# Optimization experiments

Measured on AMD Instinct MI355X. Metric: run time of the kernel, lower is better.

Reference implementation:

```python
import jax, jax.numpy as jnp
import numpy as np

N_LAYERS = 3
N_NODES = 512
D_IN = 4  # dimensions + 1
BATCH = 131072


def _glorot(key, shape):
    fan_in, fan_out = shape[-2], shape[-1]
    lim = np.sqrt(6.0 / (fan_in + fan_out))
    return jax.random.uniform(key, shape, jnp.float32, -lim, lim)


def setup_inputs() -> dict:
    key = jax.random.key(0)
    ks = jax.random.split(key, 12)
    L, n, d = N_LAYERS, N_NODES, D_IN
    return {
        "X": jax.random.normal(ks[0], (BATCH, d), jnp.float32),
        "W_in": _glorot(ks[1], (d, n)),
        "b_in": jnp.zeros((1, n), jnp.float32),
        "Wf": _glorot(ks[2], (L, d, n)),
        "Uf": _glorot(ks[3], (L, n, n)),
        "bf": jnp.zeros((L, 1, n), jnp.float32),
        "Wu": _glorot(ks[4], (L, d, n)),
        "Uu": _glorot(ks[5], (L, n, n)),
        "bu": jnp.zeros((L, 1, n), jnp.float32),
        "Wo1": _glorot(ks[6], (L, d, n)),
        "Uo1": _glorot(ks[7], (L, n, n)),
        "bo1": jnp.zeros((L, 1, n), jnp.float32),
        "Wo2": _glorot(ks[8], (L, n, n)),
        "bo2": jnp.zeros((L, 1, n), jnp.float32),
        "W_out": _glorot(ks[9], (n, 1)),
        "b_out": jnp.zeros((1, 1), jnp.float32),
    }


def reference(X, W_in, b_in, Wf, Uf, bf, Wu, Uu, bu, Wo1, Uo1, bo1, Wo2, bo2, W_out, b_out):
    # initial dense layer with swish activation
    H = jax.nn.silu(X @ W_in + b_in)  # [B, n_nodes]
    for i in range(N_LAYERS):
        F = jax.nn.sigmoid(X @ Wf[i] + H @ Uf[i] + bf[i])
        U = jax.nn.sigmoid(X @ Wu[i] + H @ Uu[i] + bu[i])
        O1 = jnp.tanh(X @ Wo1[i] + H @ Uo1[i] + bo1[i])
        O2 = jax.nn.silu((U * O1) @ Wo2[i] + bo2[i])
        H = F * H + O2
    return jax.nn.silu(H @ W_out + b_out)  # [B, 1]
```

## Files before the change

### kernel.cpp

```cpp
#include <hip/hip_runtime.h>
#include <cstdint>
#include <cstddef>

#define NLAYERS 3
#define NN      512
#define DIN     4
#define MTILE   64
#define KAUG    544
#define LDA     552
#define WELEMS  (NN * KAUG)
#define LDS_BYTES (2 * MTILE * LDA * 2)
#define NTHREADS 1024

typedef __attribute__((ext_vector_type(8))) short short8;
typedef __attribute__((ext_vector_type(4))) float f32x4;

__device__ __forceinline__ short f2bf(float f) {
    union { float f; uint32_t u; } v; v.f = f;
    uint32_t r = v.u + 0x7fffu + ((v.u >> 16) & 1u);
    return (short)(r >> 16);
}
__device__ __forceinline__ uint32_t f2bf_pk(float lo, float hi) {
    uint32_t r;
    asm("v_cvt_pk_bf16_f32 %0, %1, %2" : "=v"(r) : "v"(lo), "v"(hi));
    return r;
}
__device__ __forceinline__ float bf2f(short s) {
    union { uint32_t u; float f; } v; v.u = ((uint32_t)(uint16_t)s) << 16;
    return v.f;
}
__device__ __forceinline__ float sig_(float x)  { return 1.0f / (1.0f + __expf(-x)); }
__device__ __forceinline__ float tanh_(float x) { return 1.0f - 2.0f / (1.0f + __expf(2.0f * x)); }
__device__ __forceinline__ float silu_(float x) { return x / (1.0f + __expf(-x)); }

__device__ __forceinline__ void sig2_(float a, float b, float& sa, float& sb) {
    float da = 1.0f + __expf(-a);
    float db = 1.0f + __expf(-b);
    float inv = 1.0f / (da * db);
    sa = db * inv;
    sb = da * inv;
}
__device__ __forceinline__ void tanh2_(float a, float b, float& ta, float& tb) {
    float da = 1.0f + __expf(2.0f * a);
    float db = 1.0f + __expf(2.0f * b);
    float inv = 1.0f / (da * db);
    ta = 1.0f - 2.0f * (db * inv);
    tb = 1.0f - 2.0f * (da * inv);
}
__device__ __forceinline__ void silu2_(float a, float b, float& sa, float& sb) {
    float da = 1.0f + __expf(-a);
    float db = 1.0f + __expf(-b);
    float inv = 1.0f / (da * db);
    sa = a * (db * inv);
    sb = b * (da * inv);
}

#define MFMA_BF16 __builtin_amdgcn_mfma_f32_16x16x32_bf16

__global__ void prep_kernel(const float* __restrict__ Wf,  const float* __restrict__ Uf,  const float* __restrict__ bf,
                            const float* __restrict__ Wu,  const float* __restrict__ Uu,  const float* __restrict__ bu,
                            const float* __restrict__ Wo1, const float* __restrict__ Uo1, const float* __restrict__ bo1,
                            const float* __restrict__ Wo2, const float* __restrict__ bo2,
                            short* __restrict__ ws) {
    int idx = blockIdx.x * 256 + threadIdx.x;
    int m   = idx / WELEMS;
    if (m >= 12) return;
    int rem = idx - m * WELEMS;
    int n   = rem / KAUG;
    int kk  = rem - n * KAUG;
    int layer = m >> 2, t = m & 3;
    const float* U; const float* W; const float* b;
    switch (t) {
        case 0:  U = Uf;  W = Wf;      b = bf;  break;
        case 1:  U = Uu;  W = Wu;      b = bu;  break;
        case 2:  U = Uo1; W = Wo1;     b = bo1; break;
        default: U = Wo2; W = nullptr; b = bo2; break;
    }
    float val = 0.0f;
    if (kk < NN)             val = U[layer * NN * NN + kk * NN + n];
    else if (kk < NN + DIN)  val = W ? W[layer * DIN * NN + (kk - NN) * NN + n] : 0.0f;
    else if (kk == NN + DIN) val = b[layer * NN + n];
    ws[idx] = f2bf(val);
}

__device__ __forceinline__ void mm1(const short* __restrict__ Asrc, const short* __restrict__ Bt,
                                    int n0, int l16, int quad, f32x4 (&acc)[4][2]) {
#pragma unroll
    for (int mt = 0; mt < 4; ++mt)
#pragma unroll
        for (int nt = 0; nt < 2; ++nt) acc[mt][nt] = f32x4{0.f, 0.f, 0.f, 0.f};
    const short* aP = Asrc + l16 * LDA + quad * 8;
    const short* bP = Bt + (size_t)(n0 + l16) * KAUG + quad * 8;

    short8 a0[4], a1[4];
    short8 b0[2], b1[2];

#pragma unroll
    for (int mt = 0; mt < 4; ++mt) a0[mt] = *(const short8*)(aP + mt * 16 * LDA);
#pragma unroll
    for (int nt = 0; nt < 2; ++nt) {
        b0[nt] = *(const short8*)(bP + nt * 16 * KAUG);
        b1[nt] = *(const short8*)(bP + nt * 16 * KAUG + 32);
    }

#pragma unroll 1
    for (int i = 0; i < 7; ++i) {
#pragma unroll
        for (int mt = 0; mt < 4; ++mt) a1[mt] = *(const short8*)(aP + mt * 16 * LDA + 32);
#pragma unroll
        for (int mt = 0; mt < 4; ++mt) {
            acc[mt][0] = MFMA_BF16(a0[mt], b0[0], acc[mt][0], 0, 0, 0);
            acc[mt][1] = MFMA_BF16(a0[mt], b0[1], acc[mt][1], 0, 0, 0);
        }
#pragma unroll
        for (int nt = 0; nt < 2; ++nt) b0[nt] = *(const short8*)(bP + nt * 16 * KAUG + 64);
#pragma unroll
        for (int mt = 0; mt < 4; ++mt) a0[mt] = *(const short8*)(aP + mt * 16 * LDA + 64);
#pragma unroll
        for (int mt = 0; mt < 4; ++mt) {
            acc[mt][0] = MFMA_BF16(a1[mt], b1[0], acc[mt][0], 0, 0, 0);
            acc[mt][1] = MFMA_BF16(a1[mt], b1[1], acc[mt][1], 0, 0, 0);
        }
#pragma unroll
        for (int nt = 0; nt < 2; ++nt) b1[nt] = *(const short8*)(bP + nt * 16 * KAUG + 96);
        aP += 64; bP += 64;
    }
#pragma unroll
    for (int mt = 0; mt < 4; ++mt) a1[mt] = *(const short8*)(aP + mt * 16 * LDA + 32);
#pragma unroll
    for (int mt = 0; mt < 4; ++mt) {
        acc[mt][0] = MFMA_BF16(a0[mt], b0[0], acc[mt][0], 0, 0, 0);
        acc[mt][1] = MFMA_BF16(a0[mt], b0[1], acc[mt][1], 0, 0, 0);
    }
#pragma unroll
    for (int nt = 0; nt < 2; ++nt) b0[nt] = *(const short8*)(bP + nt * 16 * KAUG + 64);
#pragma unroll
    for (int mt = 0; mt < 4; ++mt) a0[mt] = *(const short8*)(aP + mt * 16 * LDA + 64);
#pragma unroll
    for (int mt = 0; mt < 4; ++mt) {
        acc[mt][0] = MFMA_BF16(a1[mt], b1[0], acc[mt][0], 0, 0, 0);
        acc[mt][1] = MFMA_BF16(a1[mt], b1[1], acc[mt][1], 0, 0, 0);
    }
#pragma unroll
    for (int mt = 0; mt < 4; ++mt) {
        acc[mt][0] = MFMA_BF16(a0[mt], b0[0], acc[mt][0], 0, 0, 0);
        acc[mt][1] = MFMA_BF16(a0[mt], b0[1], acc[mt][1], 0, 0, 0);
    }
}

__global__ void __launch_bounds__(NTHREADS, 4)
dgm_kernel(const float* __restrict__ X, const float* __restrict__ W_in, const float* __restrict__ b_in,
           const float* __restrict__ W_out, const float* __restrict__ b_out,
           const short* __restrict__ wmats, float* __restrict__ out) {
    extern __shared__ short lds[];
    short* Hb = lds;
    short* Tb = lds + MTILE * LDA;

    const int tid  = threadIdx.x;
    const int lane = tid & 63;
    const int wv   = tid >> 6;
    const int l16  = lane & 15;
    const int quad = lane >> 4;
    const int n0   = wv * 32;
    const int rbase = blockIdx.x * MTILE;

    {
        const int cfix = tid & (NN - 1);
        const int rstart = tid >> 9;
        const float w0 = W_in[0 * NN + cfix];
        const float w1 = W_in[1 * NN + cfix];
        const float w2 = W_in[2 * NN + cfix];
        const float w3 = W_in[3 * NN + cfix];
        const float bc = b_in[cfix];
#pragma unroll 4
        for (int j = 0; j < (MTILE * NN) / NTHREADS; ++j) {
            int r = rstart + j * (NTHREADS / NN);
            const float4 x = *(const float4*)(X + (size_t)(rbase + r) * DIN);
            float v = bc + x.x * w0 + x.y * w1 + x.z * w2 + x.w * w3;
            Hb[r * LDA + cfix] = f2bf(silu_(v));
        }
    }
    if (tid < MTILE) {
        int r = tid;
        const float* xr = X + (size_t)(rbase + r) * DIN;
#pragma unroll
        for (int k = 0; k < DIN; ++k) {
            Hb[r * LDA + NN + k] = f2bf(xr[k]);
            Tb[r * LDA + NN + k] = 0;
        }
        Hb[r * LDA + NN + DIN] = f2bf(1.0f);
        Tb[r * LDA + NN + DIN] = f2bf(1.0f);
        for (int k = NN + DIN + 1; k < KAUG; ++k) {
            Hb[r * LDA + k] = 0;
            Tb[r * LDA + k] = 0;
        }
    }
    __syncthreads();

    uint32_t Fpack[16];

    for (int layer = 0; layer < NLAYERS; ++layer) {
        const short* wF  = wmats + (size_t)(layer * 4 + 0) * WELEMS;
        const short* wU  = wmats + (size_t)(layer * 4 + 1) * WELEMS;
        const short* wO1 = wmats + (size_t)(layer * 4 + 2) * WELEMS;
        const short* wO2 = wmats + (size_t)(layer * 4 + 3) * WELEMS;

        uint32_t Tpack[16];
        {
            f32x4 aO[4][2];
            mm1(Hb, wO1, n0, l16, quad, aO);
#pragma unroll
            for (int mt = 0; mt < 4; ++mt)
#pragma unroll
                for (int nt = 0; nt < 2; ++nt)
#pragma unroll
                    for (int rp = 0; rp < 2; ++rp) {
                        float t0, t1;
                        tanh2_(aO[mt][nt][2 * rp + 0], aO[mt][nt][2 * rp + 1], t0, t1);
                        Tpack[mt * 4 + nt * 2 + rp] = f2bf_pk(t0, t1);
                    }
        }
        {
            f32x4 aU[4][2];
            mm1(Hb, wU, n0, l16, quad, aU);
#pragma unroll
            for (int mt = 0; mt < 4; ++mt)
#pragma unroll
                for (int nt = 0; nt < 2; ++nt)
#pragma unroll
                    for (int rp = 0; rp < 2; ++rp) {
                        uint32_t tp = Tpack[mt * 4 + nt * 2 + rp];
                        float to0 = bf2f((short)(uint16_t)(tp & 0xffffu));
                        float to1 = bf2f((short)(uint16_t)(tp >> 16));
                        float s0, s1;
                        sig2_(aU[mt][nt][2 * rp + 0], aU[mt][nt][2 * rp + 1], s0, s1);
                        uint32_t pk = f2bf_pk(s0 * to0, s1 * to1);
                        int row = mt * 16 + quad * 4 + 2 * rp;
                        int col = n0 + nt * 16 + l16;
                        Tb[row * LDA + col]       = (short)(uint16_t)(pk & 0xffffu);
                        Tb[(row + 1) * LDA + col] = (short)(uint16_t)(pk >> 16);
                    }
        }
        {
            f32x4 aF[4][2];
            mm1(Hb, wF, n0, l16, quad, aF);
#pragma unroll
            for (int mt = 0; mt < 4; ++mt)
#pragma unroll
                for (int nt = 0; nt < 2; ++nt)
#pragma unroll
                    for (int rp = 0; rp < 2; ++rp) {
                        float s0, s1;
                        sig2_(aF[mt][nt][2 * rp + 0], aF[mt][nt][2 * rp + 1], s0, s1);
                        Fpack[mt * 4 + nt * 2 + rp] = f2bf_pk(s0, s1);
                    }
        }
        __syncthreads();

        {
            f32x4 aO2[4][2];
            mm1(Tb, wO2, n0, l16, quad, aO2);
#pragma unroll
            for (int mt = 0; mt < 4; ++mt)
#pragma unroll
                for (int nt = 0; nt < 2; ++nt)
#pragma unroll
                    for (int rp = 0; rp < 2; ++rp) {
                        uint32_t fp = Fpack[mt * 4 + nt * 2 + rp];
                        float f0 = bf2f((short)(uint16_t)(fp & 0xffffu));
                        float f1 = bf2f((short)(uint16_t)(fp >> 16));
                        int row = mt * 16 + quad * 4 + 2 * rp;
                        int col = n0 + nt * 16 + l16;
                        float h0 = bf2f(Hb[row * LDA + col]);
                        float h1 = bf2f(Hb[(row + 1) * LDA + col]);
                        float sl0, sl1;
                        silu2_(aO2[mt][nt][2 * rp + 0], aO2[mt][nt][2 * rp + 1], sl0, sl1);
                        uint32_t pk = f2bf_pk(f0 * h0 + sl0, f1 * h1 + sl1);
                        Hb[row * LDA + col]       = (short)(uint16_t)(pk & 0xffffu);
                        Hb[(row + 1) * LDA + col] = (short)(uint16_t)(pk >> 16);
                    }
        }
        __syncthreads();
    }

    {
        const int r = tid >> 4, q = tid & 15;
        const int c0 = q * (NN / 16);
        const short8* hp = (const short8*)(Hb + r * LDA + c0);
        float p = 0.0f;
#pragma unroll
        for (int v = 0; v < (NN / 16) / 8; ++v) {
            short8 h = hp[v];
#pragma unroll
            for (int e = 0; e < 8; ++e)
                p += bf2f(h[e]) * W_out[c0 + v * 8 + e];
        }
        float* red = (float*)Tb;
        red[tid] = p;
        __syncthreads();
        if (q == 0) {
            float s = b_out[0];
#pragma unroll
            for (int i = 0; i < 16; ++i) s += red[r * 16 + i];
            out[rbase + r] = silu_(s);
        }
    }
}

extern "C" void kernel_launch(void* const* d_in, const int* in_sizes, int n_in,
                              void* d_out, int out_size, void* d_ws, size_t ws_size,
                              hipStream_t stream) {
    const float* X     = (const float*)d_in[0];
    const float* W_in  = (const float*)d_in[1];
    const float* b_in  = (const float*)d_in[2];
    const float* Wf    = (const float*)d_in[3];
    const float* Uf    = (const float*)d_in[4];
    const float* bf    = (const float*)d_in[5];
    const float* Wu    = (const float*)d_in[6];
    const float* Uu    = (const float*)d_in[7];
    const float* bu    = (const float*)d_in[8];
    const float* Wo1   = (const float*)d_in[9];
    const float* Uo1   = (const float*)d_in[10];
    const float* bo1   = (const float*)d_in[11];
    const float* Wo2   = (const float*)d_in[12];
    const float* bo2   = (const float*)d_in[13];
    const float* W_out = (const float*)d_in[14];
    const float* b_out = (const float*)d_in[15];
    float* out = (float*)d_out;
    short* ws  = (short*)d_ws;

    const int B = in_sizes[0] / DIN;

    prep_kernel<<<(12 * WELEMS + 255) / 256, 256, 0, stream>>>(
        Wf, Uf, bf, Wu, Uu, bu, Wo1, Uo1, bo1, Wo2, bo2, ws);

    hipFuncSetAttribute((const void*)dgm_kernel,
                        hipFuncAttributeMaxDynamicSharedMemorySize, LDS_BYTES);
    dgm_kernel<<<B / MTILE, NTHREADS, LDS_BYTES, stream>>>(X, W_in, b_in, W_out, b_out, ws, out);
}
```

Baseline: 1.197 ms.

## Split fused DGM kernel into per-layer global-memory GEMM kernels without LDS

Replaces the single fused kernel, which kept the H and T tiles in LDS, with a sequence of kernels: an H init kernel, three GEMM kernels per layer (U/O1 gate, F gate, O2 plus state update) and an output kernel. Activations now travel through bf16 global buffers in the workspace, and A operands are read straight from global memory. Without LDS, each kernel can have higher occupancy (launch bounds of 4). The cost is heavy extra global traffic for activations, many more kernel launches, and a dependence on the workspace size, with the old fused kernel kept as a fallback.

After: 1.177 ms. Within noise of the previous version (-1.6%).

```diff
diff --git a/kernel.cpp b/kernel.cpp
--- a/kernel.cpp
+++ b/kernel.cpp
@@ -7,6 +7,7 @@
 #define DIN     4
 #define MTILE   64
 #define KAUG    544
+#define KA      560
 #define LDA     552
 #define WELEMS  (NN * KAUG)
 #define LDS_BYTES (2 * MTILE * LDA * 2)
@@ -32,27 +33,23 @@
 __device__ __forceinline__ float sig_(float x)  { return 1.0f / (1.0f + __expf(-x)); }
 __device__ __forceinline__ float tanh_(float x) { return 1.0f - 2.0f / (1.0f + __expf(2.0f * x)); }
 __device__ __forceinline__ float silu_(float x) { return x / (1.0f + __expf(-x)); }
-
 __device__ __forceinline__ void sig2_(float a, float b, float& sa, float& sb) {
     float da = 1.0f + __expf(-a);
     float db = 1.0f + __expf(-b);
     float inv = 1.0f / (da * db);
-    sa = db * inv;
-    sb = da * inv;
+    sa = db * inv; sb = da * inv;
 }
 __device__ __forceinline__ void tanh2_(float a, float b, float& ta, float& tb) {
     float da = 1.0f + __expf(2.0f * a);
     float db = 1.0f + __expf(2.0f * b);
     float inv = 1.0f / (da * db);
-    ta = 1.0f - 2.0f * (db * inv);
-    tb = 1.0f - 2.0f * (da * inv);
+    ta = 1.0f - 2.0f * (db * inv); tb = 1.0f - 2.0f * (da * inv);
 }
 __device__ __forceinline__ void silu2_(float a, float b, float& sa, float& sb) {
     float da = 1.0f + __expf(-a);
     float db = 1.0f + __expf(-b);
     float inv = 1.0f / (da * db);
-    sa = a * (db * inv);
-    sb = b * (da * inv);
+    sa = a * (db * inv); sb = b * (da * inv);
 }
 
 #define MFMA_BF16 __builtin_amdgcn_mfma_f32_16x16x32_bf16
@@ -81,6 +78,290 @@
     else if (kk < NN + DIN)  val = W ? W[layer * DIN * NN + (kk - NN) * NN + n] : 0.0f;
     else if (kk == NN + DIN) val = b[layer * NN + n];
     ws[idx] = f2bf(val);
+}
+
+
+__device__ __forceinline__ void mm1g(const short* __restrict__ Asrc, const short* __restrict__ Bt,
+                                     int n0, int l16, int quad, f32x4 (&acc)[4][2]) {
+#pragma unroll
+    for (int mt = 0; mt < 4; ++mt)
+#pragma unroll
+        for (int nt = 0; nt < 2; ++nt) acc[mt][nt] = f32x4{0.f, 0.f, 0.f, 0.f};
+    const short* aP = Asrc + l16 * KA + quad * 8;
+    const short* bP = Bt + (size_t)(n0 + l16) * KAUG + quad * 8;
+
+    short8 a0[4], a1[4];
+    short8 b0[2], b1[2];
+
+#pragma unroll
+    for (int mt = 0; mt < 4; ++mt) a0[mt] = *(const short8*)(aP + mt * 16 * KA);
+#pragma unroll
+    for (int nt = 0; nt < 2; ++nt) {
+        b0[nt] = *(const short8*)(bP + nt * 16 * KAUG);
+        b1[nt] = *(const short8*)(bP + nt * 16 * KAUG + 32);
+    }
+
+#pragma unroll 1
+    for (int i = 0; i < 7; ++i) {
+#pragma unroll
+        for (int mt = 0; mt < 4; ++mt) a1[mt] = *(const short8*)(aP + mt * 16 * KA + 32);
+#pragma unroll
+        for (int mt = 0; mt < 4; ++mt) {
+            acc[mt][0] = MFMA_BF16(a0[mt], b0[0], acc[mt][0], 0, 0, 0);
+            acc[mt][1] = MFMA_BF16(a0[mt], b0[1], acc[mt][1], 0, 0, 0);
+        }
+#pragma unroll
+        for (int nt = 0; nt < 2; ++nt) b0[nt] = *(const short8*)(bP + nt * 16 * KAUG + 64);
+#pragma unroll
+        for (int mt = 0; mt < 4; ++mt) a0[mt] = *(const short8*)(aP + mt * 16 * KA + 64);
+#pragma unroll
+        for (int mt = 0; mt < 4; ++mt) {
+            acc[mt][0] = MFMA_BF16(a1[mt], b1[0], acc[mt][0], 0, 0, 0);
+            acc[mt][1] = MFMA_BF16(a1[mt], b1[1], acc[mt][1], 0, 0, 0);
+        }
+#pragma unroll
+        for (int nt = 0; nt < 2; ++nt) b1[nt] = *(const short8*)(bP + nt * 16 * KAUG + 96);
+        aP += 64; bP += 64;
+    }
+#pragma unroll
+    for (int mt = 0; mt < 4; ++mt) a1[mt] = *(const short8*)(aP + mt * 16 * KA + 32);
+#pragma unroll
+    for (int mt = 0; mt < 4; ++mt) {
+        acc[mt][0] = MFMA_BF16(a0[mt], b0[0], acc[mt][0], 0, 0, 0);
+        acc[mt][1] = MFMA_BF16(a0[mt], b0[1], acc[mt][1], 0, 0, 0);
+    }
+#pragma unroll
+    for (int nt = 0; nt < 2; ++nt) b0[nt] = *(const short8*)(bP + nt * 16 * KAUG + 64);
+#pragma unroll
+    for (int mt = 0; mt < 4; ++mt) a0[mt] = *(const short8*)(aP + mt * 16 * KA + 64);
+#pragma unroll
+    for (int mt = 0; mt < 4; ++mt) {
+        acc[mt][0] = MFMA_BF16(a1[mt], b1[0], acc[mt][0], 0, 0, 0);
+        acc[mt][1] = MFMA_BF16(a1[mt], b1[1], acc[mt][1], 0, 0, 0);
+    }
+#pragma unroll
+    for (int mt = 0; mt < 4; ++mt) {
+        acc[mt][0] = MFMA_BF16(a0[mt], b0[0], acc[mt][0], 0, 0, 0);
+        acc[mt][1] = MFMA_BF16(a0[mt], b0[1], acc[mt][1], 0, 0, 0);
+    }
+}
+
+__device__ __forceinline__ void mmUO1g(const short* __restrict__ Asrc,
+                                       const short* __restrict__ BtU, const short* __restrict__ BtO,
+                                       int n0, int l16, int quad,
+                                       f32x4 (&accU)[4][2], f32x4 (&accO)[4][2]) {
+#pragma unroll
+    for (int mt = 0; mt < 4; ++mt)
+#pragma unroll
+        for (int nt = 0; nt < 2; ++nt) {
+            accU[mt][nt] = f32x4{0.f, 0.f, 0.f, 0.f};
+            accO[mt][nt] = f32x4{0.f, 0.f, 0.f, 0.f};
+        }
+    const short* aP  = Asrc + l16 * KA + quad * 8;
+    const short* bUP = BtU + (size_t)(n0 + l16) * KAUG + quad * 8;
+    const short* bOP = BtO + (size_t)(n0 + l16) * KAUG + quad * 8;
+
+    short8 a[4];
+    short8 bU0[2], bU1[2], bO0[2], bO1[2];
+
+#pragma unroll
+    for (int mt = 0; mt < 4; ++mt) a[mt] = *(const short8*)(aP + mt * 16 * KA);
+#pragma unroll
+    for (int nt = 0; nt < 2; ++nt) {
+        bU0[nt] = *(const short8*)(bUP + nt * 16 * KAUG);
+        bU1[nt] = *(const short8*)(bUP + nt * 16 * KAUG + 32);
+        bO0[nt] = *(const short8*)(bOP + nt * 16 * KAUG);
+        bO1[nt] = *(const short8*)(bOP + nt * 16 * KAUG + 32);
+    }
+
+#pragma unroll 1
+    for (int i = 0; i < 8; ++i) {
+#pragma unroll
+        for (int mt = 0; mt < 4; ++mt) {
+            accU[mt][0] = MFMA_BF16(a[mt], bU0[0], accU[mt][0], 0, 0, 0);
+            accU[mt][1] = MFMA_BF16(a[mt], bU0[1], accU[mt][1], 0, 0, 0);
+            accO[mt][0] = MFMA_BF16(a[mt], bO0[0], accO[mt][0], 0, 0, 0);
+            accO[mt][1] = MFMA_BF16(a[mt], bO0[1], accO[mt][1], 0, 0, 0);
+            a[mt] = *(const short8*)(aP + mt * 16 * KA + 32);
+        }
+#pragma unroll
+        for (int nt = 0; nt < 2; ++nt) {
+            bU0[nt] = *(const short8*)(bUP + nt * 16 * KAUG + 64);
+            bO0[nt] = *(const short8*)(bOP + nt * 16 * KAUG + 64);
+        }
+#pragma unroll
+        for (int mt = 0; mt < 4; ++mt) {
+            accU[mt][0] = MFMA_BF16(a[mt], bU1[0], accU[mt][0], 0, 0, 0);
+            accU[mt][1] = MFMA_BF16(a[mt], bU1[1], accU[mt][1], 0, 0, 0);
+            accO[mt][0] = MFMA_BF16(a[mt], bO1[0], accO[mt][0], 0, 0, 0);
+            accO[mt][1] = MFMA_BF16(a[mt], bO1[1], accO[mt][1], 0, 0, 0);
+            a[mt] = *(const short8*)(aP + mt * 16 * KA + 64);
+        }
+#pragma unroll
+        for (int nt = 0; nt < 2; ++nt) {
+            bU1[nt] = *(const short8*)(bUP + nt * 16 * KAUG + 96);
+            bO1[nt] = *(const short8*)(bOP + nt * 16 * KAUG + 96);
+        }
+        aP += 64; bUP += 64; bOP += 64;
+    }
+#pragma unroll
+    for (int mt = 0; mt < 4; ++mt) {
+        accU[mt][0] = MFMA_BF16(a[mt], bU0[0], accU[mt][0], 0, 0, 0);
+        accU[mt][1] = MFMA_BF16(a[mt], bU0[1], accU[mt][1], 0, 0, 0);
+        accO[mt][0] = MFMA_BF16(a[mt], bO0[0], accO[mt][0], 0, 0, 0);
+        accO[mt][1] = MFMA_BF16(a[mt], bO0[1], accO[mt][1], 0, 0, 0);
+    }
+}
+
+__global__ void __launch_bounds__(NTHREADS)
+hinit_kernel(const float* __restrict__ X, const float* __restrict__ W_in, const float* __restrict__ b_in,
+             short* __restrict__ Hg, short* __restrict__ Tg) {
+    const int tid = threadIdx.x;
+    const int rbase = blockIdx.x * MTILE;
+    {
+        const int cfix = tid & (NN - 1);
+        const int rstart = tid >> 9;
+        const float w0 = W_in[0 * NN + cfix];
+        const float w1 = W_in[1 * NN + cfix];
+        const float w2 = W_in[2 * NN + cfix];
+        const float w3 = W_in[3 * NN + cfix];
+        const float bc = b_in[cfix];
+#pragma unroll 4
+        for (int j = 0; j < (MTILE * NN) / NTHREADS; ++j) {
+            int r = rstart + j * (NTHREADS / NN);
+            const float4 x = *(const float4*)(X + (size_t)(rbase + r) * DIN);
+            float v = bc + x.x * w0 + x.y * w1 + x.z * w2 + x.w * w3;
+            Hg[(size_t)(rbase + r) * KA + cfix] = f2bf(silu_(v));
+        }
+    }
+    if (tid < MTILE) {
+        int r = rbase + tid;
+        const float* xr = X + (size_t)r * DIN;
+#pragma unroll
+        for (int k = 0; k < DIN; ++k) {
+            Hg[(size_t)r * KA + NN + k] = f2bf(xr[k]);
+            Tg[(size_t)r * KA + NN + k] = 0;
+        }
+        Hg[(size_t)r * KA + NN + DIN] = f2bf(1.0f);
+        Tg[(size_t)r * KA + NN + DIN] = f2bf(1.0f);
+        for (int k = NN + DIN + 1; k < KAUG; ++k) {
+            Hg[(size_t)r * KA + k] = 0;
+            Tg[(size_t)r * KA + k] = 0;
+        }
+    }
+}
+
+__global__ void __launch_bounds__(NTHREADS, 4)
+gemm_t_kernel(const short* __restrict__ Hg, const short* __restrict__ wU, const short* __restrict__ wO1,
+              short* __restrict__ Tg) {
+    const int tid  = threadIdx.x;
+    const int lane = tid & 63;
+    const int wv   = tid >> 6;
+    const int l16  = lane & 15;
+    const int quad = lane >> 4;
+    const int n0   = wv * 32;
+    const int rbase = blockIdx.x * MTILE;
+
+    f32x4 aU[4][2], aO[4][2];
+    mmUO1g(Hg + (size_t)rbase * KA, wU, wO1, n0, l16, quad, aU, aO);
+#pragma unroll
+    for (int mt = 0; mt < 4; ++mt)
+#pragma unroll
+        for (int nt = 0; nt < 2; ++nt)
+#pragma unroll
+            for (int rp = 0; rp < 2; ++rp) {
+                float t0, t1, s0, s1;
+                tanh2_(aO[mt][nt][2 * rp + 0], aO[mt][nt][2 * rp + 1], t0, t1);
+                sig2_(aU[mt][nt][2 * rp + 0], aU[mt][nt][2 * rp + 1], s0, s1);
+                uint32_t pk = f2bf_pk(s0 * t0, s1 * t1);
+                int row = rbase + mt * 16 + quad * 4 + 2 * rp;
+                int col = n0 + nt * 16 + l16;
+                Tg[(size_t)row * KA + col]       = (short)(uint16_t)(pk & 0xffffu);
+                Tg[(size_t)(row + 1) * KA + col] = (short)(uint16_t)(pk >> 16);
+            }
+}
+
+__global__ void __launch_bounds__(NTHREADS, 4)
+gemm_f_kernel(const short* __restrict__ Hg, const short* __restrict__ wF, short* __restrict__ Fg) {
+    const int tid  = threadIdx.x;
+    const int lane = tid & 63;
+    const int wv   = tid >> 6;
+    const int l16  = lane & 15;
+    const int quad = lane >> 4;
+    const int n0   = wv * 32;
+    const int rbase = blockIdx.x * MTILE;
+
+    f32x4 aF[4][2];
+    mm1g(Hg + (size_t)rbase * KA, wF, n0, l16, quad, aF);
+#pragma unroll
+    for (int mt = 0; mt < 4; ++mt)
+#pragma unroll
+        for (int nt = 0; nt < 2; ++nt)
+#pragma unroll
+            for (int rp = 0; rp < 2; ++rp) {
+                float s0, s1;
+                sig2_(aF[mt][nt][2 * rp + 0], aF[mt][nt][2 * rp + 1], s0, s1);
+                uint32_t pk = f2bf_pk(s0, s1);
+                int row = rbase + mt * 16 + quad * 4 + 2 * rp;
+                int col = n0 + nt * 16 + l16;
+                Fg[(size_t)row * NN + col]       = (short)(uint16_t)(pk & 0xffffu);
+                Fg[(size_t)(row + 1) * NN + col] = (short)(uint16_t)(pk >> 16);
+            }
+}
+
+__global__ void __launch_bounds__(NTHREADS, 4)
+gemm_h_kernel(const short* __restrict__ Tg, const short* __restrict__ wO2,
+              const short* __restrict__ Fg, short* __restrict__ Hg) {
+    const int tid  = threadIdx.x;
+    const int lane = tid & 63;
+    const int wv   = tid >> 6;
+    const int l16  = lane & 15;
+    const int quad = lane >> 4;
+    const int n0   = wv * 32;
+    const int rbase = blockIdx.x * MTILE;
+
+    f32x4 aO2[4][2];
+    mm1g(Tg + (size_t)rbase * KA, wO2, n0, l16, quad, aO2);
+#pragma unroll
+    for (int mt = 0; mt < 4; ++mt)
+#pragma unroll
+        for (int nt = 0; nt < 2; ++nt)
+#pragma unroll
+            for (int rp = 0; rp < 2; ++rp) {
+                int row = rbase + mt * 16 + quad * 4 + 2 * rp;
+                int col = n0 + nt * 16 + l16;
+                float f0 = bf2f(Fg[(size_t)row * NN + col]);
+                float f1 = bf2f(Fg[(size_t)(row + 1) * NN + col]);
+                float h0 = bf2f(Hg[(size_t)row * KA + col]);
+                float h1 = bf2f(Hg[(size_t)(row + 1) * KA + col]);
+                float sl0, sl1;
+                silu2_(aO2[mt][nt][2 * rp + 0], aO2[mt][nt][2 * rp + 1], sl0, sl1);
+                uint32_t pk = f2bf_pk(f0 * h0 + sl0, f1 * h1 + sl1);
+                Hg[(size_t)row * KA + col]       = (short)(uint16_t)(pk & 0xffffu);
+                Hg[(size_t)(row + 1) * KA + col] = (short)(uint16_t)(pk >> 16);
+            }
+}
+
+__global__ void __launch_bounds__(NTHREADS)
+out_kernel(const short* __restrict__ Hg, const float* __restrict__ W_out, const float* __restrict__ b_out,
+           float* __restrict__ outp) {
+    const int tid = threadIdx.x;
+    const int q = tid & 15;
+    const int row = blockIdx.x * MTILE + (tid >> 4);
+    const short8* hp = (const short8*)(Hg + (size_t)row * KA + q * 32);
+    float p = 0.0f;
+#pragma unroll
+    for (int v = 0; v < 4; ++v) {
+        short8 h = hp[v];
+#pragma unroll
+        for (int e = 0; e < 8; ++e)
+            p += bf2f(h[e]) * W_out[q * 32 + v * 8 + e];
+    }
+    p += __shfl_xor(p, 8, 16);
+    p += __shfl_xor(p, 4, 16);
+    p += __shfl_xor(p, 2, 16);
+    p += __shfl_xor(p, 1, 16);
+    if (q == 0) outp[row] = silu_(p + b_out[0]);
 }
 
 __device__ __forceinline__ void mm1(const short* __restrict__ Asrc, const short* __restrict__ Bt,
@@ -334,7 +615,28 @@
     prep_kernel<<<(12 * WELEMS + 255) / 256, 256, 0, stream>>>(
         Wf, Uf, bf, Wu, Uu, bu, Wo1, Uo1, bo1, Wo2, bo2, ws);
 
-    hipFuncSetAttribute((const void*)dgm_kernel,
-                        hipFuncAttributeMaxDynamicSharedMemorySize, LDS_BYTES);
-    dgm_kernel<<<B / MTILE, NTHREADS, LDS_BYTES, stream>>>(X, W_in, b_in, W_out, b_out, ws, out);
-}
+    const size_t need = 2ull * (12ull * WELEMS + 2ull * (size_t)B * KA + (size_t)B * NN);
+
+    if (ws_size >= need && (B % MTILE) == 0) {
+        short* Hg = ws + 12ull * WELEMS;
+        short* Tg = Hg + (size_t)B * KA;
+        short* Fg = Tg + (size_t)B * KA;
+        const int G = B / MTILE;
+
+        hinit_kernel<<<G, NTHREADS, 0, stream>>>(X, W_in, b_in, Hg, Tg);
+        for (int layer = 0; layer < NLAYERS; ++layer) {
+            const short* wF  = ws + (size_t)(layer * 4 + 0) * WELEMS;
+            const short* wU  = ws + (size_t)(layer * 4 + 1) * WELEMS;
+            const short* wO1 = ws + (size_t)(layer * 4 + 2) * WELEMS;
+            const short* wO2 = ws + (size_t)(layer * 4 + 3) * WELEMS;
+            gemm_t_kernel<<<G, NTHREADS, 0, stream>>>(Hg, wU, wO1, Tg);
+            gemm_f_kernel<<<G, NTHREADS, 0, stream>>>(Hg, wF, Fg);
+            gemm_h_kernel<<<G, NTHREADS, 0, stream>>>(Tg, wO2, Fg, Hg);
+        }
+        out_kernel<<<G, NTHREADS, 0, stream>>>(Hg, W_out, b_out, out);
+    } else {
+        hipFuncSetAttribute((const void*)dgm_kernel,
+                            hipFuncAttributeMaxDynamicSharedMemorySize, LDS_BYTES);
+        dgm_kernel<<<B / MTILE, NTHREADS, LDS_BYTES, stream>>>(X, W_in, b_in, W_out, b_out, ws, out);
+    }
+}
```

## Halve row tile to 32 with 8 waves each covering 64 output columns

Applied to the files above, without the earlier changes.

Shrinks the per-block row tile from 64 to 32 and the block from 1024 to 512 threads, so each wave now computes 32 rows by 64 columns instead of 64 rows by 32. This halves LDS per block and doubles the grid, which may raise occupancy. Each wave now loads more weight fragments from global/L2 per MFMA (4 B tiles per 2 A tiles). Total weight traffic doubles because twice as many blocks each stream all layer weights.

Result: slower. 1.811 ms (+51.4%).

```diff
diff --git a/kernel.cpp b/kernel.cpp
--- a/kernel.cpp
+++ b/kernel.cpp
@@ -5,12 +5,12 @@
 #define NLAYERS 3
 #define NN      512
 #define DIN     4
-#define MTILE   64
+#define MTILE   32
 #define KAUG    544
 #define LDA     552
 #define WELEMS  (NN * KAUG)
 #define LDS_BYTES (2 * MTILE * LDA * 2)
-#define NTHREADS 1024
+#define NTHREADS 512
 
 typedef __attribute__((ext_vector_type(8))) short short8;
 typedef __attribute__((ext_vector_type(4))) float f32x4;
@@ -32,27 +32,23 @@
 __device__ __forceinline__ float sig_(float x)  { return 1.0f / (1.0f + __expf(-x)); }
 __device__ __forceinline__ float tanh_(float x) { return 1.0f - 2.0f / (1.0f + __expf(2.0f * x)); }
 __device__ __forceinline__ float silu_(float x) { return x / (1.0f + __expf(-x)); }
-
 __device__ __forceinline__ void sig2_(float a, float b, float& sa, float& sb) {
     float da = 1.0f + __expf(-a);
     float db = 1.0f + __expf(-b);
     float inv = 1.0f / (da * db);
-    sa = db * inv;
-    sb = da * inv;
+    sa = db * inv; sb = da * inv;
 }
 __device__ __forceinline__ void tanh2_(float a, float b, float& ta, float& tb) {
     float da = 1.0f + __expf(2.0f * a);
     float db = 1.0f + __expf(2.0f * b);
     float inv = 1.0f / (da * db);
-    ta = 1.0f - 2.0f * (db * inv);
-    tb = 1.0f - 2.0f * (da * inv);
+    ta = 1.0f - 2.0f * (db * inv); tb = 1.0f - 2.0f * (da * inv);
 }
 __device__ __forceinline__ void silu2_(float a, float b, float& sa, float& sb) {
     float da = 1.0f + __expf(-a);
     float db = 1.0f + __expf(-b);
     float inv = 1.0f / (da * db);
-    sa = a * (db * inv);
-    sb = b * (da * inv);
+    sa = a * (db * inv); sb = b * (da * inv);
 }
 
 #define MFMA_BF16 __builtin_amdgcn_mfma_f32_16x16x32_bf16
@@ -84,21 +80,21 @@
 }
 
 __device__ __forceinline__ void mm1(const short* __restrict__ Asrc, const short* __restrict__ Bt,
-                                    int n0, int l16, int quad, f32x4 (&acc)[4][2]) {
-#pragma unroll
-    for (int mt = 0; mt < 4; ++mt)
-#pragma unroll
-        for (int nt = 0; nt < 2; ++nt) acc[mt][nt] = f32x4{0.f, 0.f, 0.f, 0.f};
+                                    int n0, int l16, int quad, f32x4 (&acc)[2][4]) {
+#pragma unroll
+    for (int mt = 0; mt < 2; ++mt)
+#pragma unroll
+        for (int nt = 0; nt < 4; ++nt) acc[mt][nt] = f32x4{0.f, 0.f, 0.f, 0.f};
     const short* aP = Asrc + l16 * LDA + quad * 8;
     const short* bP = Bt + (size_t)(n0 + l16) * KAUG + quad * 8;
 
-    short8 a0[4], a1[4];
-    short8 b0[2], b1[2];
-
-#pragma unroll
-    for (int mt = 0; mt < 4; ++mt) a0[mt] = *(const short8*)(aP + mt * 16 * LDA);
-#pragma unroll
-    for (int nt = 0; nt < 2; ++nt) {
+    short8 a0[2], a1[2];
+    short8 b0[4], b1[4];
+
+#pragma unroll
+    for (int mt = 0; mt < 2; ++mt) a0[mt] = *(const short8*)(aP + mt * 16 * LDA);
+#pragma unroll
+    for (int nt = 0; nt < 4; ++nt) {
         b0[nt] = *(const short8*)(bP + nt * 16 * KAUG);
         b1[nt] = *(const short8*)(bP + nt * 16 * KAUG + 32);
     }
@@ -106,46 +102,46 @@
 #pragma unroll 1
     for (int i = 0; i < 7; ++i) {
 #pragma unroll
-        for (int mt = 0; mt < 4; ++mt) a1[mt] = *(const short8*)(aP + mt * 16 * LDA + 32);
-#pragma unroll
-        for (int mt = 0; mt < 4; ++mt) {
-            acc[mt][0] = MFMA_BF16(a0[mt], b0[0], acc[mt][0], 0, 0, 0);
-            acc[mt][1] = MFMA_BF16(a0[mt], b0[1], acc[mt][1], 0, 0, 0);
-        }
-#pragma unroll
-        for (int nt = 0; nt < 2; ++nt) b0[nt] = *(const short8*)(bP + nt * 16 * KAUG + 64);
-#pragma unroll
-        for (int mt = 0; mt < 4; ++mt) a0[mt] = *(const short8*)(aP + mt * 16 * LDA + 64);
-#pragma unroll
-        for (int mt = 0; mt < 4; ++mt) {
-            acc[mt][0] = MFMA_BF16(a1[mt], b1[0], acc[mt][0], 0, 0, 0);
-            acc[mt][1] = MFMA_BF16(a1[mt], b1[1], acc[mt][1], 0, 0, 0);
-        }
-#pragma unroll
-        for (int nt = 0; nt < 2; ++nt) b1[nt] = *(const short8*)(bP + nt * 16 * KAUG + 96);
+        for (int mt = 0; mt < 2; ++mt) a1[mt] = *(const short8*)(aP + mt * 16 * LDA + 32);
+#pragma unroll
+        for (int mt = 0; mt < 2; ++mt)
+#pragma unroll
+            for (int nt = 0; nt < 4; ++nt)
+                acc[mt][nt] = MFMA_BF16(a0[mt], b0[nt], acc[mt][nt], 0, 0, 0);
+#pragma unroll
+        for (int nt = 0; nt < 4; ++nt) b0[nt] = *(const short8*)(bP + nt * 16 * KAUG + 64);
+#pragma unroll
+        for (int mt = 0; mt < 2; ++mt) a0[mt] = *(const short8*)(aP + mt * 16 * LDA + 64);
+#pragma unroll
+        for (int mt = 0; mt < 2; ++mt)
+#pragma unroll
+            for (int nt = 0; nt < 4; ++nt)
+                acc[mt][nt] = MFMA_BF16(a1[mt], b1[nt], acc[mt][nt], 0, 0, 0);
+#pragma unroll
+        for (int nt = 0; nt < 4; ++nt) b1[nt] = *(const short8*)(bP + nt * 16 * KAUG + 96);
         aP += 64; bP += 64;
     }
 #pragma unroll
-    for (int mt = 0; mt < 4; ++mt) a1[mt] = *(const short8*)(aP + mt * 16 * LDA + 32);
-#pragma unroll
-    for (int mt = 0; mt < 4; ++mt) {
-        acc[mt][0] = MFMA_BF16(a0[mt], b0[0], acc[mt][0], 0, 0, 0);
-        acc[mt][1] = MFMA_BF16(a0[mt], b0[1], acc[mt][1], 0, 0, 0);
-    }
-#pragma unroll
-    for (int nt = 0; nt < 2; ++nt) b0[nt] = *(const short8*)(bP + nt * 16 * KAUG + 64);
-#pragma unroll
-    for (int mt = 0; mt < 4; ++mt) a0[mt] = *(const short8*)(aP + mt * 16 * LDA + 64);
-#pragma unroll
-    for (int mt = 0; mt < 4; ++mt) {
-        acc[mt][0] = MFMA_BF16(a1[mt], b1[0], acc[mt][0], 0, 0, 0);
-        acc[mt][1] = MFMA_BF16(a1[mt], b1[1], acc[mt][1], 0, 0, 0);
-    }
-#pragma unroll
-    for (int mt = 0; mt < 4; ++mt) {
-        acc[mt][0] = MFMA_BF16(a0[mt], b0[0], acc[mt][0], 0, 0, 0);
-        acc[mt][1] = MFMA_BF16(a0[mt], b0[1], acc[mt][1], 0, 0, 0);
-    }
+    for (int mt = 0; mt < 2; ++mt) a1[mt] = *(const short8*)(aP + mt * 16 * LDA + 32);
+#pragma unroll
+    for (int mt = 0; mt < 2; ++mt)
+#pragma unroll
+        for (int nt = 0; nt < 4; ++nt)
+            acc[mt][nt] = MFMA_BF16(a0[mt], b0[nt], acc[mt][nt], 0, 0, 0);
+#pragma unroll
+    for (int nt = 0; nt < 4; ++nt) b0[nt] = *(const short8*)(bP + nt * 16 * KAUG + 64);
+#pragma unroll
+    for (int mt = 0; mt < 2; ++mt) a0[mt] = *(const short8*)(aP + mt * 16 * LDA + 64);
+#pragma unroll
+    for (int mt = 0; mt < 2; ++mt)
+#pragma unroll
+        for (int nt = 0; nt < 4; ++nt)
+            acc[mt][nt] = MFMA_BF16(a1[mt], b1[nt], acc[mt][nt], 0, 0, 0);
+#pragma unroll
+    for (int mt = 0; mt < 2; ++mt)
+#pragma unroll
+        for (int nt = 0; nt < 4; ++nt)
+            acc[mt][nt] = MFMA_BF16(a0[mt], b0[nt], acc[mt][nt], 0, 0, 0);
 }
 
 __global__ void __launch_bounds__(NTHREADS, 4)
@@ -161,20 +157,18 @@
     const int wv   = tid >> 6;
     const int l16  = lane & 15;
     const int quad = lane >> 4;
-    const int n0   = wv * 32;
+    const int n0   = wv * 64;
     const int rbase = blockIdx.x * MTILE;
 
     {
         const int cfix = tid & (NN - 1);
-        const int rstart = tid >> 9;
         const float w0 = W_in[0 * NN + cfix];
         const float w1 = W_in[1 * NN + cfix];
         const float w2 = W_in[2 * NN + cfix];
         const float w3 = W_in[3 * NN + cfix];
         const float bc = b_in[cfix];
 #pragma unroll 4
-        for (int j = 0; j < (MTILE * NN) / NTHREADS; ++j) {
-            int r = rstart + j * (NTHREADS / NN);
+        for (int r = 0; r < MTILE; ++r) {
             const float4 x = *(const float4*)(X + (size_t)(rbase + r) * DIN);
             float v = bc + x.x * w0 + x.y * w1 + x.z * w2 + x.w * w3;
             Hb[r * LDA + cfix] = f2bf(silu_(v));
@@ -207,29 +201,29 @@
 
         uint32_t Tpack[16];
         {
-            f32x4 aO[4][2];
+            f32x4 aO[2][4];
             mm1(Hb, wO1, n0, l16, quad, aO);
 #pragma unroll
-            for (int mt = 0; mt < 4; ++mt)
-#pragma unroll
-                for (int nt = 0; nt < 2; ++nt)
+            for (int mt = 0; mt < 2; ++mt)
+#pragma unroll
+                for (int nt = 0; nt < 4; ++nt)
 #pragma unroll
                     for (int rp = 0; rp < 2; ++rp) {
                         float t0, t1;
                         tanh2_(aO[mt][nt][2 * rp + 0], aO[mt][nt][2 * rp + 1], t0, t1);
-                        Tpack[mt * 4 + nt * 2 + rp] = f2bf_pk(t0, t1);
+                        Tpack[mt * 8 + nt * 2 + rp] = f2bf_pk(t0, t1);
                     }
         }
         {
-            f32x4 aU[4][2];
+            f32x4 aU[2][4];
             mm1(Hb, wU, n0, l16, quad, aU);
 #pragma unroll
-            for (int mt = 0; mt < 4; ++mt)
-#pragma unroll
-                for (int nt = 0; nt < 2; ++nt)
+            for (int mt = 0; mt < 2; ++mt)
+#pragma unroll
+                for (int nt = 0; nt < 4; ++nt)
 #pragma unroll
                     for (int rp = 0; rp < 2; ++rp) {
-                        uint32_t tp = Tpack[mt * 4 + nt * 2 + rp];
+                        uint32_t tp = Tpack[mt * 8 + nt * 2 + rp];
                         float to0 = bf2f((short)(uint16_t)(tp & 0xffffu));
                         float to1 = bf2f((short)(uint16_t)(tp >> 16));
                         float s0, s1;
@@ -242,31 +236,31 @@
                     }
         }
         {
-            f32x4 aF[4][2];
+            f32x4 aF[2][4];
             mm1(Hb, wF, n0, l16, quad, aF);
 #pragma unroll
-            for (int mt = 0; mt < 4; ++mt)
-#pragma unroll
-                for (int nt = 0; nt < 2; ++nt)
+            for (int mt = 0; mt < 2; ++mt)
+#pragma unroll
+                for (int nt = 0; nt < 4; ++nt)
 #pragma unroll
                     for (int rp = 0; rp < 2; ++rp) {
                         float s0, s1;
                         sig2_(aF[mt][nt][2 * rp + 0], aF[mt][nt][2 * rp + 1], s0, s1);
-                        Fpack[mt * 4 + nt * 2 + rp] = f2bf_pk(s0, s1);
+                        Fpack[mt * 8 + nt * 2 + rp] = f2bf_pk(s0, s1);
                     }
         }
         __syncthreads();
 
         {
-            f32x4 aO2[4][2];
+            f32x4 aO2[2][4];
             mm1(Tb, wO2, n0, l16, quad, aO2);
 #pragma unroll
-            for (int mt = 0; mt < 4; ++mt)
-#pragma unroll
-                for (int nt = 0; nt < 2; ++nt)
+            for (int mt = 0; mt < 2; ++mt)
+#pragma unroll
+                for (int nt = 0; nt < 4; ++nt)
 #pragma unroll
                     for (int rp = 0; rp < 2; ++rp) {
-                        uint32_t fp = Fpack[mt * 4 + nt * 2 + rp];
+                        uint32_t fp = Fpack[mt * 8 + nt * 2 + rp];
                         float f0 = bf2f((short)(uint16_t)(fp & 0xffffu));
                         float f1 = bf2f((short)(uint16_t)(fp >> 16));
                         int row = mt * 16 + quad * 4 + 2 * rp;
```
